# Kernel optimization log

Measured on AMD Instinct MI355X. Metric: run time of the kernel, lower is better.

## Reference

```python
import jax, jax.numpy as jnp
import numpy as np
jax.config.update("jax_enable_x64", True)

T, C, F = 2048, 2048, 8192
f32 = jnp.float32
f64 = jnp.float64


def setup_inputs() -> dict:
    key = jax.random.key(0)
    ks = jax.random.split(key, 20)
    s = 0.02
    return {
        "x": jax.random.normal(ks[0], (T, C), f32),
        "att_shift": jnp.zeros((C,), f32),
        "wkv_state": jnp.zeros((2, C), f32),
        "ffn_shift": jnp.zeros((C,), f32),
        "ln1_w": jnp.ones((C,), f32),
        "ln1_b": jnp.zeros((C,), f32),
        "ln2_w": jnp.ones((C,), f32),
        "ln2_b": jnp.zeros((C,), f32),
        "time_mix_k": jax.random.uniform(ks[1], (C,), f32),
        "time_mix_v": jax.random.uniform(ks[2], (C,), f32),
        "time_mix_r": jax.random.uniform(ks[3], (C,), f32),
        "time_decay": jax.random.normal(ks[4], (C,), f32) * 0.5,
        "time_first": jax.random.normal(ks[5], (C,), f32) * 0.5,
        "att_key": jax.random.normal(ks[6], (C, C), f32) * s,
        "att_value": jax.random.normal(ks[7], (C, C), f32) * s,
        "att_receptance": jax.random.normal(ks[8], (C, C), f32) * s,
        "att_output": jax.random.normal(ks[9], (C, C), f32) * s,
        "ffn_time_mix_k": jax.random.uniform(ks[10], (C,), f32),
        "ffn_time_mix_r": jax.random.uniform(ks[11], (C,), f32),
        "ffn_key": jax.random.normal(ks[12], (F, C), f32) * s,
        "ffn_value": jax.random.normal(ks[13], (C, F), f32) * s,
        "ffn_receptance": jax.random.normal(ks[14], (C, C), f32) * s,
    }


def _ln(x, w, b):
    m = x.mean(-1, keepdims=True)
    v = x.var(-1, keepdims=True)
    return (x - m) * jax.lax.rsqrt(v + 1e-5) * w + b


def _wkv(time_decay, time_first, k, v, wkv_state):
    # faithful to wkv_mop: double-precision math, float32 state round-trip per step
    u = time_first.astype(f64)
    w = -jnp.exp(time_decay.astype(f64))
    ew = jnp.exp(w)

    def step(carry, kv_t):
        a, b = carry  # float32 states [C]
        k_t, v_t = kv_t
        kd = k_t.astype(f64)
        vd = v_t.astype(f64)
        e = jnp.exp(u + w + kd)
        y = (a + e * vd) / (b + e)
        kk = jnp.exp(kd)
        a2 = ((a + kk * vd) * ew).astype(f32)
        b2 = ((b + kk) * ew).astype(f32)
        return (a2, b2), y.astype(f32)

    _, y = jax.lax.scan(step, (wkv_state[0], wkv_state[1]), (k, v))
    return y  # [T, C]


def reference(x, att_shift, wkv_state, ffn_shift, ln1_w, ln1_b, ln2_w, ln2_b,
              time_mix_k, time_mix_v, time_mix_r, time_decay, time_first,
              att_key, att_value, att_receptance, att_output,
              ffn_time_mix_k, ffn_time_mix_r, ffn_key, ffn_value, ffn_receptance):
    # --- TimeMix (att) on rx = ln1(x); shiftamount=2 -> prev token of rx ---
    rx = _ln(x, ln1_w, ln1_b)                         # [T, C]
    xx = jnp.concatenate([att_shift[None, :], rx[:-1]], axis=0)
    xk = rx * time_mix_k + xx * (1.0 - time_mix_k)
    xv = rx * time_mix_v + xx * (1.0 - time_mix_v)
    xr = rx * time_mix_r + xx * (1.0 - time_mix_r)
    k = xk @ att_key.T                                # [T, C]
    v = xv @ att_value.T
    sr = jax.nn.sigmoid(xr @ att_receptance.T)
    y = _wkv(time_decay, time_first, k, v, wkv_state)
    x = x + (sr * y) @ att_output.T
    # --- ChannelMix (ffn) on fx = ln2(x); shift = prev token of fx ---
    fx = _ln(x, ln2_w, ln2_b)
    fxx = jnp.concatenate([ffn_shift[None, :], fx[:-1]], axis=0)
    fk = fx * ffn_time_mix_k + fxx * (1.0 - ffn_time_mix_k)
    fr = fx * ffn_time_mix_r + fxx * (1.0 - ffn_time_mix_r)
    kf = jnp.square(jax.nn.relu(fk @ ffn_key.T))      # [T, F]
    kv = kf @ ffn_value.T                             # [T, C]
    out = x + jax.nn.sigmoid(fr @ ffn_receptance.T) * kv
    return out
```

## Files before the change

kernel.cpp:

```cpp
#include <hip/hip_runtime.h>
#include <hip/hip_bf16.h>

typedef unsigned short u16;
typedef short bf16x8 __attribute__((ext_vector_type(8)));
typedef float f32x4 __attribute__((ext_vector_type(4)));

#define T_DIM 2048
#define C_DIM 2048
#define F_DIM 8192
#define WKV_L 32
#define WKV_P (T_DIM / WKV_L)

__device__ __forceinline__ u16 f2bf(float f) {
    unsigned int u = __float_as_uint(f);
    u += 0x7fff + ((u >> 16) & 1);
    return (u16)(u >> 16);
}

__device__ __forceinline__ void async16(const void* g, void* l) {
    __builtin_amdgcn_global_load_lds(
        (__attribute__((address_space(1))) const unsigned int*)g,
        (__attribute__((address_space(3))) unsigned int*)l, 16, 0, 0);
}

__global__ __launch_bounds__(256) void ln_mix3(
        const float* __restrict__ x, const float* __restrict__ sh,
        const float* __restrict__ w, const float* __restrict__ b,
        const float* __restrict__ mk, const float* __restrict__ mv,
        const float* __restrict__ mr,
        u16* __restrict__ xk, u16* __restrict__ xv, u16* __restrict__ xr) {
    __shared__ float red[16];
    const int t = blockIdx.x, tid = threadIdx.x;
    const float4* cr = (const float4*)(x + (size_t)t * C_DIM);
    float4 c0 = cr[tid * 2], c1 = cr[tid * 2 + 1];
    float s = c0.x + c0.y + c0.z + c0.w + c1.x + c1.y + c1.z + c1.w;
    float q = c0.x * c0.x + c0.y * c0.y + c0.z * c0.z + c0.w * c0.w
            + c1.x * c1.x + c1.y * c1.y + c1.z * c1.z + c1.w * c1.w;
    float4 p0, p1;
    float sp = 0.f, qp = 0.f;
    if (t > 0) {
        const float4* pr = (const float4*)(x + (size_t)(t - 1) * C_DIM);
        p0 = pr[tid * 2]; p1 = pr[tid * 2 + 1];
        sp = p0.x + p0.y + p0.z + p0.w + p1.x + p1.y + p1.z + p1.w;
        qp = p0.x * p0.x + p0.y * p0.y + p0.z * p0.z + p0.w * p0.w
           + p1.x * p1.x + p1.y * p1.y + p1.z * p1.z + p1.w * p1.w;
    } else {
        const float4* pr = (const float4*)sh;
        p0 = pr[tid * 2]; p1 = pr[tid * 2 + 1];
    }
    #pragma unroll
    for (int off = 32; off > 0; off >>= 1) {
        s += __shfl_down(s, off);   q += __shfl_down(q, off);
        sp += __shfl_down(sp, off); qp += __shfl_down(qp, off);
    }
    const int lane = tid & 63, wv = tid >> 6;
    if (lane == 0) { red[wv] = s; red[4 + wv] = q; red[8 + wv] = sp; red[12 + wv] = qp; }
    __syncthreads();
    if (tid == 0) {
        red[0] += red[1] + red[2] + red[3];
        red[4] += red[5] + red[6] + red[7];
        red[8] += red[9] + red[10] + red[11];
        red[12] += red[13] + red[14] + red[15];
    }
    __syncthreads();
    const float mc = red[0] * (1.f / C_DIM);
    const float ic = rsqrtf(red[4] * (1.f / C_DIM) - mc * mc + 1e-5f);
    const float mp = red[8] * (1.f / C_DIM);
    const float ip = rsqrtf(red[12] * (1.f / C_DIM) - mp * mp + 1e-5f);
    const float4* w4 = (const float4*)w;
    const float4* b4 = (const float4*)b;
    #pragma unroll
    for (int j = 0; j < 2; ++j) {
        const int i4 = tid * 2 + j;
        float4 cv = j ? c1 : c0, pv = j ? p1 : p0;
        float4 wv4 = w4[i4], bv = b4[i4];
        float4 cl, pl;
        cl.x = (cv.x - mc) * ic * wv4.x + bv.x;
        cl.y = (cv.y - mc) * ic * wv4.y + bv.y;
        cl.z = (cv.z - mc) * ic * wv4.z + bv.z;
        cl.w = (cv.w - mc) * ic * wv4.w + bv.w;
        if (t > 0) {
            pl.x = (pv.x - mp) * ip * wv4.x + bv.x;
            pl.y = (pv.y - mp) * ip * wv4.y + bv.y;
            pl.z = (pv.z - mp) * ip * wv4.z + bv.z;
            pl.w = (pv.w - mp) * ip * wv4.w + bv.w;
        } else pl = pv;
        const size_t o = (size_t)t * (C_DIM / 4) + i4;
        float4 m;
        ushort4 r;
        m = ((const float4*)mk)[i4];
        r.x = f2bf(cl.x * m.x + pl.x * (1.f - m.x));
        r.y = f2bf(cl.y * m.y + pl.y * (1.f - m.y));
        r.z = f2bf(cl.z * m.z + pl.z * (1.f - m.z));
        r.w = f2bf(cl.w * m.w + pl.w * (1.f - m.w));
        ((ushort4*)xk)[o] = r;
        m = ((const float4*)mv)[i4];
        r.x = f2bf(cl.x * m.x + pl.x * (1.f - m.x));
        r.y = f2bf(cl.y * m.y + pl.y * (1.f - m.y));
        r.z = f2bf(cl.z * m.z + pl.z * (1.f - m.z));
        r.w = f2bf(cl.w * m.w + pl.w * (1.f - m.w));
        ((ushort4*)xv)[o] = r;
        m = ((const float4*)mr)[i4];
        r.x = f2bf(cl.x * m.x + pl.x * (1.f - m.x));
        r.y = f2bf(cl.y * m.y + pl.y * (1.f - m.y));
        r.z = f2bf(cl.z * m.z + pl.z * (1.f - m.z));
        r.w = f2bf(cl.w * m.w + pl.w * (1.f - m.w));
        ((ushort4*)xr)[o] = r;
    }
}

__global__ __launch_bounds__(256) void ln_mix2(
        const float* __restrict__ x, const float* __restrict__ sh,
        const float* __restrict__ w, const float* __restrict__ b,
        const float* __restrict__ mk, const float* __restrict__ mr,
        u16* __restrict__ fk, u16* __restrict__ fr) {
    __shared__ float red[16];
    const int t = blockIdx.x, tid = threadIdx.x;
    const float4* cr = (const float4*)(x + (size_t)t * C_DIM);
    float4 c0 = cr[tid * 2], c1 = cr[tid * 2 + 1];
    float s = c0.x + c0.y + c0.z + c0.w + c1.x + c1.y + c1.z + c1.w;
    float q = c0.x * c0.x + c0.y * c0.y + c0.z * c0.z + c0.w * c0.w
            + c1.x * c1.x + c1.y * c1.y + c1.z * c1.z + c1.w * c1.w;
    float4 p0, p1;
    float sp = 0.f, qp = 0.f;
    if (t > 0) {
        const float4* pr = (const float4*)(x + (size_t)(t - 1) * C_DIM);
        p0 = pr[tid * 2]; p1 = pr[tid * 2 + 1];
        sp = p0.x + p0.y + p0.z + p0.w + p1.x + p1.y + p1.z + p1.w;
        qp = p0.x * p0.x + p0.y * p0.y + p0.z * p0.z + p0.w * p0.w
           + p1.x * p1.x + p1.y * p1.y + p1.z * p1.z + p1.w * p1.w;
    } else {
        const float4* pr = (const float4*)sh;
        p0 = pr[tid * 2]; p1 = pr[tid * 2 + 1];
    }
    #pragma unroll
    for (int off = 32; off > 0; off >>= 1) {
        s += __shfl_down(s, off);   q += __shfl_down(q, off);
        sp += __shfl_down(sp, off); qp += __shfl_down(qp, off);
    }
    const int lane = tid & 63, wv = tid >> 6;
    if (lane == 0) { red[wv] = s; red[4 + wv] = q; red[8 + wv] = sp; red[12 + wv] = qp; }
    __syncthreads();
    if (tid == 0) {
        red[0] += red[1] + red[2] + red[3];
        red[4] += red[5] + red[6] + red[7];
        red[8] += red[9] + red[10] + red[11];
        red[12] += red[13] + red[14] + red[15];
    }
    __syncthreads();
    const float mc = red[0] * (1.f / C_DIM);
    const float ic = rsqrtf(red[4] * (1.f / C_DIM) - mc * mc + 1e-5f);
    const float mp = red[8] * (1.f / C_DIM);
    const float ip = rsqrtf(red[12] * (1.f / C_DIM) - mp * mp + 1e-5f);
    const float4* w4 = (const float4*)w;
    const float4* b4 = (const float4*)b;
    #pragma unroll
    for (int j = 0; j < 2; ++j) {
        const int i4 = tid * 2 + j;
        float4 cv = j ? c1 : c0, pv = j ? p1 : p0;
        float4 wv4 = w4[i4], bv = b4[i4];
        float4 cl, pl;
        cl.x = (cv.x - mc) * ic * wv4.x + bv.x;
        cl.y = (cv.y - mc) * ic * wv4.y + bv.y;
        cl.z = (cv.z - mc) * ic * wv4.z + bv.z;
        cl.w = (cv.w - mc) * ic * wv4.w + bv.w;
        if (t > 0) {
            pl.x = (pv.x - mp) * ip * wv4.x + bv.x;
            pl.y = (pv.y - mp) * ip * wv4.y + bv.y;
            pl.z = (pv.z - mp) * ip * wv4.z + bv.z;
            pl.w = (pv.w - mp) * ip * wv4.w + bv.w;
        } else pl = pv;
        const size_t o = (size_t)t * (C_DIM / 4) + i4;
        float4 m;
        ushort4 r;
        m = ((const float4*)mk)[i4];
        r.x = f2bf(cl.x * m.x + pl.x * (1.f - m.x));
        r.y = f2bf(cl.y * m.y + pl.y * (1.f - m.y));
        r.z = f2bf(cl.z * m.z + pl.z * (1.f - m.z));
        r.w = f2bf(cl.w * m.w + pl.w * (1.f - m.w));
        ((ushort4*)fk)[o] = r;
        m = ((const float4*)mr)[i4];
        r.x = f2bf(cl.x * m.x + pl.x * (1.f - m.x));
        r.y = f2bf(cl.y * m.y + pl.y * (1.f - m.y));
        r.z = f2bf(cl.z * m.z + pl.z * (1.f - m.z));
        r.w = f2bf(cl.w * m.w + pl.w * (1.f - m.w));
        ((ushort4*)fr)[o] = r;
    }
}

__global__ __launch_bounds__(256) void cvt_bf16(const float* __restrict__ in,
                                                u16* __restrict__ out, int n8) {
    int i = blockIdx.x * 256 + threadIdx.x;
    const int stride = gridDim.x * 256;
    for (; i < n8; i += stride) {
        const float4* p = (const float4*)(in + (size_t)i * 8);
        float4 a = p[0], b = p[1];
        ushort4 lo, hi;
        lo.x = f2bf(a.x); lo.y = f2bf(a.y); lo.z = f2bf(a.z); lo.w = f2bf(a.w);
        hi.x = f2bf(b.x); hi.y = f2bf(b.y); hi.z = f2bf(b.z); hi.w = f2bf(b.w);
        ((ushort4*)out)[i * 2] = lo;
        ((ushort4*)out)[i * 2 + 1] = hi;
    }
}

__global__ __launch_bounds__(256) void cvt3_bf16(const float* __restrict__ i0,
                                                 const float* __restrict__ i1,
                                                 const float* __restrict__ i2,
                                                 u16* __restrict__ out, int n8) {
    const int sel = blockIdx.y;
    const float* in = sel == 0 ? i0 : (sel == 1 ? i1 : i2);
    u16* o = out + (size_t)sel * n8 * 8;
    int i = blockIdx.x * 256 + threadIdx.x;
    const int stride = gridDim.x * 256;
    for (; i < n8; i += stride) {
        const float4* p = (const float4*)(in + (size_t)i * 8);
        float4 a = p[0], b = p[1];
        ushort4 lo, hi;
        lo.x = f2bf(a.x); lo.y = f2bf(a.y); lo.z = f2bf(a.z); lo.w = f2bf(a.w);
        hi.x = f2bf(b.x); hi.y = f2bf(b.y); hi.z = f2bf(b.z); hi.w = f2bf(b.w);
        ((ushort4*)o)[i * 2] = lo;
        ((ushort4*)o)[i * 2 + 1] = hi;
    }
}

__global__ __launch_bounds__(256) void wkv_part(const float* __restrict__ td,
                                                const float* __restrict__ k,
                                                const float* __restrict__ v,
                                                float* __restrict__ Ab,
                                                float* __restrict__ Bb) {
    const int idx = blockIdx.x * 256 + threadIdx.x;
    const int c = idx & (C_DIM - 1);
    const int p = idx >> 11;
    const float ew = expf(-expf(td[c]));
    float A = 0.f, B = 0.f;
    size_t o = (size_t)(p * WKV_L) * C_DIM + c;
    #pragma unroll 4
    for (int i = 0; i < WKV_L; ++i, o += C_DIM) {
        const float kk = expf(k[o]);
        A = (A + kk * v[o]) * ew;
        B = (B + kk) * ew;
    }
    Ab[p * C_DIM + c] = A;
    Bb[p * C_DIM + c] = B;
}

__global__ __launch_bounds__(256) void wkv_comb(const float* __restrict__ td,
                                                const float* __restrict__ st,
                                                const float* __restrict__ Ab,
                                                const float* __restrict__ Bb,
                                                float* __restrict__ Sa,
                                                float* __restrict__ Sb) {
    const int c = blockIdx.x * 256 + threadIdx.x;
    const float w = -expf(td[c]);
    const float dL = expf(w * (float)WKV_L);
    float a = st[c];
    float b = st[C_DIM + c];
    #pragma unroll 4
    for (int p = 0; p < WKV_P; ++p) {
        Sa[p * C_DIM + c] = a;
        Sb[p * C_DIM + c] = b;
        a = dL * a + Ab[p * C_DIM + c];
        b = dL * b + Bb[p * C_DIM + c];
    }
}

__global__ __launch_bounds__(256) void wkv_emit(const float* __restrict__ td,
                                                const float* __restrict__ tf,
                                                const float* __restrict__ k,
                                                const float* __restrict__ v,
                                                const float* __restrict__ r,
                                                const float* __restrict__ Sa,
                                                const float* __restrict__ Sb,
                                                u16* __restrict__ pout) {
    const int idx = blockIdx.x * 256 + threadIdx.x;
    const int c = idx & (C_DIM - 1);
    const int p = idx >> 11;
    const float u = tf[c];
    const float w = -expf(td[c]);
    const float ew = expf(w);
    float a = Sa[p * C_DIM + c];
    float b = Sb[p * C_DIM + c];
    size_t o = (size_t)(p * WKV_L) * C_DIM + c;
    #pragma unroll 2
    for (int i = 0; i < WKV_L; ++i, o += C_DIM) {
        const float kt = k[o], vt = v[o], rt = r[o];
        const float e = expf(u + w + kt);
        const float y = (a + e * vt) / (b + e);
        const float kk = expf(kt);
        a = (a + kk * vt) * ew;
        b = (b + kk) * ew;
        const float sr = 1.f / (1.f + expf(-rt));
        pout[o] = f2bf(sr * y);
    }
}

enum { EPI_F32 = 0, EPI_ADDX = 1, EPI_RELU2 = 2, EPI_SIGMULADD4 = 3 };

template <int EPI>
__global__ __launch_bounds__(512, 2) void gemm256(
        const u16* __restrict__ A, int lda, long a_zs,
        const u16* __restrict__ B, int ldb, long b_zs,
        int Kloop,
        void* __restrict__ outp, int ldo, long o_zs,
        const float* __restrict__ aux1, const float* __restrict__ aux2) {
    __shared__ u16 lds[4 * 16384];
    const int tid = threadIdx.x;
    const int l = tid & 63, w = tid >> 6;
    const int wr = w >> 2, wcn = w & 3;

    const int gx = gridDim.x, gy = gridDim.y;
    const int nxy = gx * gy;
    const int flat = (blockIdx.z * gy + blockIdx.y) * gx + blockIdx.x;
    const int cpx = (nxy * gridDim.z) >> 3;
    const int swz = (flat & 7) * cpx + (flat >> 3);
    const int z = swz / nxy;
    const int rem = swz - z * nxy;
    const int bm = rem % gy;
    const int bn = rem / gy;

    const u16* Ag = A + (size_t)z * a_zs + (size_t)bm * 256 * lda;
    const u16* Bg = B + (size_t)z * b_zs + (size_t)bn * 256 * ldb;

    long gA[2], gB[2];
    int dA[2], dB[2];
    #pragma unroll
    for (int j = 0; j < 2; ++j) {
        const int off = j * 8192 + w * 1024 + l * 16;
        const int row = off >> 6;
        const int cb = (off & 63) ^ (((off >> 9) & 1) << 5);
        gA[j] = (long)row * lda + (cb >> 1);
        gB[j] = (long)row * ldb + (cb >> 1);
        dA[j] = j * 4096 + w * 512;
        dB[j] = 8192 + j * 4096 + w * 512;
    }

    int offA[8], offB[4];
    #pragma unroll
    for (int m = 0; m < 8; ++m) {
        const int lin = (wr * 128 + m * 16 + (l & 15)) * 64 + ((l >> 4) << 4);
        offA[m] = (lin ^ (((lin >> 9) & 1) << 5)) >> 1;
    }
    #pragma unroll
    for (int n = 0; n < 4; ++n) {
        const int lin = (wcn * 64 + n * 16 + (l & 15)) * 64 + ((l >> 4) << 4);
        offB[n] = 8192 + ((lin ^ (((lin >> 9) & 1) << 5)) >> 1);
    }

    const f32x4 fz = {0.f, 0.f, 0.f, 0.f};
    f32x4 acc[8][4];
    #pragma unroll
    for (int m = 0; m < 8; ++m)
        #pragma unroll
        for (int n = 0; n < 4; ++n) acc[m][n] = fz;

    const int NT = Kloop >> 5;

    auto stage = [&](int kt, int sp) {
        const long ko = (long)kt << 5;
        const int sb = sp * 16384;
        async16(Ag + gA[0] + ko, &lds[sb + dA[0]]);
        async16(Ag + gA[1] + ko, &lds[sb + dA[1]]);
        async16(Bg + gB[0] + ko, &lds[sb + dB[0]]);
        async16(Bg + gB[1] + ko, &lds[sb + dB[1]]);
    };

    stage(0, 0);
    stage(1, 1);
    stage(2, 2);

    for (int t = 0; t < NT; ++t) {
        asm volatile("s_waitcnt vmcnt(8)" ::: "memory");
        __builtin_amdgcn_s_barrier();
        __builtin_amdgcn_sched_barrier(0);
        {
            const int tp = (t + 3 < NT) ? t + 3 : NT - 1;
            stage(tp, (t + 3) & 3);
        }
        const int sb = (t & 3) * 16384;
        bf16x8 af[8], bfv[4];
        #pragma unroll
        for (int m = 0; m < 8; ++m) af[m] = *(const bf16x8*)&lds[sb + offA[m]];
        #pragma unroll
        for (int n = 0; n < 4; ++n) bfv[n] = *(const bf16x8*)&lds[sb + offB[n]];
        __builtin_amdgcn_s_setprio(1);
        #pragma unroll
        for (int m = 0; m < 4; ++m)
            #pragma unroll
            for (int n = 0; n < 4; ++n)
                acc[m][n] = __builtin_amdgcn_mfma_f32_16x16x32_bf16(af[m], bfv[n], acc[m][n], 0, 0, 0);
        __builtin_amdgcn_s_setprio(0);
        __builtin_amdgcn_s_setprio(1);
        #pragma unroll
        for (int m = 4; m < 8; ++m)
            #pragma unroll
            for (int n = 0; n < 4; ++n)
                acc[m][n] = __builtin_amdgcn_mfma_f32_16x16x32_bf16(af[m], bfv[n], acc[m][n], 0, 0, 0);
        __builtin_amdgcn_s_setprio(0);
    }
    asm volatile("s_waitcnt vmcnt(0)" ::: "memory");

    const int r00 = bm * 256 + wr * 128 + ((l >> 4) << 2);
    const int c00 = bn * 256 + wcn * 64 + (l & 15);
    #pragma unroll
    for (int m = 0; m < 8; ++m) {
        #pragma unroll
        for (int n = 0; n < 4; ++n) {
            #pragma unroll
            for (int j = 0; j < 4; ++j) {
                const int rr = r00 + m * 16 + j;
                const int cc = c00 + n * 16;
                const size_t o = (size_t)rr * ldo + cc;
                const float val = acc[m][n][j];
                if constexpr (EPI == EPI_F32) {
                    ((float*)outp)[(size_t)z * o_zs + o] = val;
                } else if constexpr (EPI == EPI_ADDX) {
                    ((float*)outp)[o] = aux1[o] + val;
                } else if constexpr (EPI == EPI_RELU2) {
                    const float tp2 = fmaxf(val, 0.f);
                    ((u16*)outp)[o] = f2bf(tp2 * tp2);
                } else {
                    const float kv = aux2[o]
                                   + aux2[o + (size_t)T_DIM * C_DIM]
                                   + aux2[o + 2 * (size_t)T_DIM * C_DIM]
                                   + aux2[o + 3 * (size_t)T_DIM * C_DIM];
                    const float sg = 1.f / (1.f + expf(-val));
                    ((float*)outp)[o] = aux1[o] + sg * kv;
                }
            }
        }
    }
}

extern "C" void kernel_launch(void* const* d_in, const int* in_sizes, int n_in,
                              void* d_out, int out_size, void* d_ws, size_t ws_size,
                              hipStream_t stream) {
    const float* x         = (const float*)d_in[0];
    const float* att_shift = (const float*)d_in[1];
    const float* wkv_state = (const float*)d_in[2];
    const float* ffn_shift = (const float*)d_in[3];
    const float* ln1w = (const float*)d_in[4];
    const float* ln1b = (const float*)d_in[5];
    const float* ln2w = (const float*)d_in[6];
    const float* ln2b = (const float*)d_in[7];
    const float* tmk  = (const float*)d_in[8];
    const float* tmv  = (const float*)d_in[9];
    const float* tmr  = (const float*)d_in[10];
    const float* td   = (const float*)d_in[11];
    const float* tf   = (const float*)d_in[12];
    const float* Wk   = (const float*)d_in[13];
    const float* Wv   = (const float*)d_in[14];
    const float* Wr   = (const float*)d_in[15];
    const float* Wo   = (const float*)d_in[16];
    const float* ftmk = (const float*)d_in[17];
    const float* ftmr = (const float*)d_in[18];
    const float* Wfk  = (const float*)d_in[19];
    const float* Wfv  = (const float*)d_in[20];
    const float* Wfr  = (const float*)d_in[21];
    float* out = (float*)d_out;

    char* ws = (char*)d_ws;
    const size_t MB = 1ull << 20;
    u16*   xk  = (u16*)(ws + 16 * MB);
    u16*   xv  = (u16*)(ws + 24 * MB);
    u16*   xr  = (u16*)(ws + 32 * MB);
    float* kb  = (float*)(ws + 40 * MB);
    float* vb  = (float*)(ws + 56 * MB);
    float* rb  = (float*)(ws + 72 * MB);
    u16*   pb  = (u16*)(ws + 88 * MB);
    float* x1  = (float*)(ws + 96 * MB);
    u16*   kf  = (u16*)(ws + 112 * MB);
    u16*   Wb  = (u16*)(ws + 144 * MB);
    float* wAb = (float*)(ws + 112 * MB);
    float* wBb = (float*)(ws + 112 * MB + 512 * 1024);
    float* wSa = (float*)(ws + 113 * MB);
    float* wSb = (float*)(ws + 113 * MB + 512 * 1024);
    float* fvp = (float*)(ws + 32 * MB);

    const int T = T_DIM, C = C_DIM, F = F_DIM;
    const dim3 blk(256), blk5(512);

    ln_mix3<<<T, blk, 0, stream>>>(x, att_shift, ln1w, ln1b, tmk, tmv, tmr, xk, xv, xr);

    cvt3_bf16<<<dim3(1024, 3), blk, 0, stream>>>(Wk, Wv, Wr, Wb, C * C / 8);
    gemm256<EPI_F32><<<dim3(C / 256, T / 256, 3), blk5, 0, stream>>>(
        xk, C, (long)T * C, Wb, C, (long)C * C, C, kb, C, (long)T * C, nullptr, nullptr);

    wkv_part<<<(C * WKV_P) / 256, blk, 0, stream>>>(td, kb, vb, wAb, wBb);
    wkv_comb<<<C / 256, blk, 0, stream>>>(td, wkv_state, wAb, wBb, wSa, wSb);
    wkv_emit<<<(C * WKV_P) / 256, blk, 0, stream>>>(td, tf, kb, vb, rb, wSa, wSb, pb);

    cvt_bf16<<<2048, blk, 0, stream>>>(Wo, Wb, C * C / 8);
    gemm256<EPI_ADDX><<<dim3(C / 256, T / 256, 1), blk5, 0, stream>>>(
        pb, C, 0, Wb, C, 0, C, x1, C, 0, x, nullptr);

    ln_mix2<<<T, blk, 0, stream>>>(x1, ffn_shift, ln2w, ln2b, ftmk, ftmr, xk, xv);

    cvt_bf16<<<2048, blk, 0, stream>>>(Wfk, Wb, F * C / 8);
    gemm256<EPI_RELU2><<<dim3(F / 256, T / 256, 1), blk5, 0, stream>>>(
        xk, C, 0, Wb, C, 0, C, kf, F, 0, nullptr, nullptr);

    cvt_bf16<<<2048, blk, 0, stream>>>(Wfv, Wb, C * F / 8);
    gemm256<EPI_F32><<<dim3(C / 256, T / 256, 4), blk5, 0, stream>>>(
        kf, F, 2048, Wb, F, 2048, 2048, fvp, C, (long)T * C, nullptr, nullptr);

    cvt_bf16<<<2048, blk, 0, stream>>>(Wfr, Wb, C * C / 8);
    gemm256<EPI_SIGMULADD4><<<dim3(C / 256, T / 256, 1), blk5, 0, stream>>>(
        xv, C, 0, Wb, C, 0, C, out, C, 0, x1, fvp);
}
```

Baseline: 451.6 us.

## Use 128x128 GEMM kernel for square projections and pre-reduce split-K partials

```diff
diff --git a/kernel.cpp b/kernel.cpp
--- a/kernel.cpp
+++ b/kernel.cpp
@@ -223,6 +223,25 @@
     }
 }
 
+__global__ __launch_bounds__(256) void reduce4(const float* __restrict__ p0,
+                                               const float* __restrict__ p1,
+                                               const float* __restrict__ p2,
+                                               const float* __restrict__ p3,
+                                               float* __restrict__ o, int n4) {
+    int i = blockIdx.x * 256 + threadIdx.x;
+    const int stride = gridDim.x * 256;
+    for (; i < n4; i += stride) {
+        float4 a = ((const float4*)p0)[i], b = ((const float4*)p1)[i];
+        float4 c = ((const float4*)p2)[i], d = ((const float4*)p3)[i];
+        float4 r;
+        r.x = a.x + b.x + c.x + d.x;
+        r.y = a.y + b.y + c.y + d.y;
+        r.z = a.z + b.z + c.z + d.z;
+        r.w = a.w + b.w + c.w + d.w;
+        ((float4*)o)[i] = r;
+    }
+}
+
 __global__ __launch_bounds__(256) void wkv_part(const float* __restrict__ td,
                                                 const float* __restrict__ k,
                                                 const float* __restrict__ v,
@@ -294,7 +313,7 @@
     }
 }
 
-enum { EPI_F32 = 0, EPI_ADDX = 1, EPI_RELU2 = 2, EPI_SIGMULADD4 = 3 };
+enum { EPI_F32 = 0, EPI_ADDX = 1, EPI_RELU2 = 2, EPI_SIGMULADD = 3 };
 
 template <int EPI>
 __global__ __launch_bounds__(512, 2) void gemm256(
@@ -413,18 +432,90 @@
                 const float val = acc[m][n][j];
                 if constexpr (EPI == EPI_F32) {
                     ((float*)outp)[(size_t)z * o_zs + o] = val;
-                } else if constexpr (EPI == EPI_ADDX) {
-                    ((float*)outp)[o] = aux1[o] + val;
-                } else if constexpr (EPI == EPI_RELU2) {
+                } else {
                     const float tp2 = fmaxf(val, 0.f);
                     ((u16*)outp)[o] = f2bf(tp2 * tp2);
+                }
+            }
+        }
+    }
+}
+
+template <int EPI>
+__global__ __launch_bounds__(256) void gemm_bt(const u16* __restrict__ A,
+                                               const u16* __restrict__ B,
+                                               int M, int N, int K,
+                                               void* __restrict__ outp,
+                                               const float* __restrict__ aux1,
+                                               const float* __restrict__ aux2) {
+    __shared__ u16 As[128 * 64];
+    __shared__ u16 Bs[128 * 64];
+    const int tid = threadIdx.x;
+    const int lane = tid & 63, wid = tid >> 6;
+    const int wr = wid >> 1, wc = wid & 1;
+    const int bm = blockIdx.y, bn = blockIdx.x;
+
+    const u16* Ag = A + (size_t)bm * 128 * K;
+    const u16* Bg = B + (size_t)bn * 128 * K;
+
+    const f32x4 fz = {0.f, 0.f, 0.f, 0.f};
+    f32x4 acc[4][4];
+    #pragma unroll
+    for (int m = 0; m < 4; ++m)
+        #pragma unroll
+        for (int n = 0; n < 4; ++n) acc[m][n] = fz;
+
+    const int nk = K >> 6;
+    for (int kt = 0; kt < nk; ++kt) {
+        const u16* Agk = Ag + (kt << 6);
+        const u16* Bgk = Bg + (kt << 6);
+        #pragma unroll
+        for (int i = 0; i < 4; ++i) {
+            const int id = i * 256 + tid;
+            async16(Agk + (size_t)(id >> 3) * K + ((id & 7) << 3), &As[(i * 4 + wid) << 9]);
+        }
+        #pragma unroll
+        for (int i = 0; i < 4; ++i) {
+            const int id = i * 256 + tid;
+            async16(Bgk + (size_t)(id >> 3) * K + ((id & 7) << 3), &Bs[(i * 4 + wid) << 9]);
+        }
+        __syncthreads();
+        #pragma unroll
+        for (int kk = 0; kk < 2; ++kk) {
+            const int ko = (kk << 5) + ((lane >> 4) << 3);
+            bf16x8 af[4], bfr[4];
+            #pragma unroll
+            for (int m = 0; m < 4; ++m)
+                af[m] = *(const bf16x8*)&As[((wr << 6) + (m << 4) + (lane & 15)) * 64 + ko];
+            #pragma unroll
+            for (int n = 0; n < 4; ++n)
+                bfr[n] = *(const bf16x8*)&Bs[((wc << 6) + (n << 4) + (lane & 15)) * 64 + ko];
+            #pragma unroll
+            for (int m = 0; m < 4; ++m)
+                #pragma unroll
+                for (int n = 0; n < 4; ++n)
+                    acc[m][n] = __builtin_amdgcn_mfma_f32_16x16x32_bf16(af[m], bfr[n], acc[m][n], 0, 0, 0);
+        }
+        __syncthreads();
+    }
+
+    const int r0 = bm * 128 + (wr << 6) + ((lane >> 4) << 2);
+    const int c0 = bn * 128 + (wc << 6) + (lane & 15);
+    #pragma unroll
+    for (int m = 0; m < 4; ++m) {
+        #pragma unroll
+        for (int n = 0; n < 4; ++n) {
+            #pragma unroll
+            for (int j = 0; j < 4; ++j) {
+                const int rr = r0 + (m << 4) + j;
+                const int cc = c0 + (n << 4);
+                const size_t o = (size_t)rr * N + cc;
+                const float val = acc[m][n][j];
+                if constexpr (EPI == EPI_ADDX) {
+                    ((float*)outp)[o] = aux1[o] + val;
                 } else {
-                    const float kv = aux2[o]
-                                   + aux2[o + (size_t)T_DIM * C_DIM]
-                                   + aux2[o + 2 * (size_t)T_DIM * C_DIM]
-                                   + aux2[o + 3 * (size_t)T_DIM * C_DIM];
                     const float sg = 1.f / (1.f + expf(-val));
-                    ((float*)outp)[o] = aux1[o] + sg * kv;
+                    ((float*)outp)[o] = aux1[o] + sg * aux2[o];
                 }
             }
         }
@@ -460,6 +551,7 @@
 
     char* ws = (char*)d_ws;
     const size_t MB = 1ull << 20;
+    float* rx0 = (float*)(ws + 0);
     u16*   xk  = (u16*)(ws + 16 * MB);
     u16*   xv  = (u16*)(ws + 24 * MB);
     u16*   xr  = (u16*)(ws + 32 * MB);
@@ -490,8 +582,8 @@
     wkv_emit<<<(C * WKV_P) / 256, blk, 0, stream>>>(td, tf, kb, vb, rb, wSa, wSb, pb);
 
     cvt_bf16<<<2048, blk, 0, stream>>>(Wo, Wb, C * C / 8);
-    gemm256<EPI_ADDX><<<dim3(C / 256, T / 256, 1), blk5, 0, stream>>>(
-        pb, C, 0, Wb, C, 0, C, x1, C, 0, x, nullptr);
+    gemm_bt<EPI_ADDX><<<dim3(C / 128, T / 128), blk, 0, stream>>>(
+        pb, Wb, T, C, C, x1, x, nullptr);
 
     ln_mix2<<<T, blk, 0, stream>>>(x1, ffn_shift, ln2w, ln2b, ftmk, ftmr, xk, xv);
 
@@ -502,8 +594,10 @@
     cvt_bf16<<<2048, blk, 0, stream>>>(Wfv, Wb, C * F / 8);
     gemm256<EPI_F32><<<dim3(C / 256, T / 256, 4), blk5, 0, stream>>>(
         kf, F, 2048, Wb, F, 2048, 2048, fvp, C, (long)T * C, nullptr, nullptr);
+    reduce4<<<2048, blk, 0, stream>>>(fvp, fvp + (size_t)T * C, fvp + 2 * (size_t)T * C,
+                                      fvp + 3 * (size_t)T * C, rx0, T * C / 4);
 
     cvt_bf16<<<2048, blk, 0, stream>>>(Wfr, Wb, C * C / 8);
-    gemm256<EPI_SIGMULADD4><<<dim3(C / 256, T / 256, 1), blk5, 0, stream>>>(
-        xv, C, 0, Wb, C, 0, C, out, C, 0, x1, fvp);
-}
+    gemm_bt<EPI_SIGMULADD><<<dim3(C / 128, T / 128), blk, 0, stream>>>(
+        xv, Wb, T, C, C, out, x1, rx0);
+}
```

Result: faster. 421.8 us (-6.6%).

## Shrink GEMM tiles to 128x128 and use two-way split-K with separate reduction

Applied to the files above, without the earlier changes.

```diff
diff --git a/kernel.cpp b/kernel.cpp
--- a/kernel.cpp
+++ b/kernel.cpp
@@ -223,6 +223,22 @@
     }
 }
 
+__global__ __launch_bounds__(256) void reduce2(const float* __restrict__ p0,
+                                               const float* __restrict__ p1,
+                                               float* __restrict__ o, int n4) {
+    int i = blockIdx.x * 256 + threadIdx.x;
+    const int stride = gridDim.x * 256;
+    for (; i < n4; i += stride) {
+        float4 a = ((const float4*)p0)[i], b = ((const float4*)p1)[i];
+        float4 r;
+        r.x = a.x + b.x;
+        r.y = a.y + b.y;
+        r.z = a.z + b.z;
+        r.w = a.w + b.w;
+        ((float4*)o)[i] = r;
+    }
+}
+
 __global__ __launch_bounds__(256) void wkv_part(const float* __restrict__ td,
                                                 const float* __restrict__ k,
                                                 const float* __restrict__ v,
@@ -294,19 +310,19 @@
     }
 }
 
-enum { EPI_F32 = 0, EPI_ADDX = 1, EPI_RELU2 = 2, EPI_SIGMULADD4 = 3 };
+enum { EPI_F32 = 0, EPI_ADDX = 1, EPI_RELU2 = 2, EPI_SIGMULADD = 3 };
 
 template <int EPI>
-__global__ __launch_bounds__(512, 2) void gemm256(
+__global__ __launch_bounds__(256, 2) void gemm_bt(
         const u16* __restrict__ A, int lda, long a_zs,
         const u16* __restrict__ B, int ldb, long b_zs,
-        int Kloop,
+        long koff, int Kloop,
         void* __restrict__ outp, int ldo, long o_zs,
         const float* __restrict__ aux1, const float* __restrict__ aux2) {
-    __shared__ u16 lds[4 * 16384];
+    __shared__ u16 lds[4 * 8192];
     const int tid = threadIdx.x;
     const int l = tid & 63, w = tid >> 6;
-    const int wr = w >> 2, wcn = w & 3;
+    const int wr2 = w >> 1, wc2 = w & 1;
 
     const int gx = gridDim.x, gy = gridDim.y;
     const int nxy = gx * gy;
@@ -318,38 +334,38 @@
     const int bm = rem % gy;
     const int bn = rem / gy;
 
-    const u16* Ag = A + (size_t)z * a_zs + (size_t)bm * 256 * lda;
-    const u16* Bg = B + (size_t)z * b_zs + (size_t)bn * 256 * ldb;
+    const u16* Ag = A + (size_t)z * a_zs + (size_t)z * koff + (size_t)bm * 128 * lda;
+    const u16* Bg = B + (size_t)z * b_zs + (size_t)z * koff + (size_t)bn * 128 * ldb;
 
     long gA[2], gB[2];
     int dA[2], dB[2];
     #pragma unroll
     for (int j = 0; j < 2; ++j) {
-        const int off = j * 8192 + w * 1024 + l * 16;
+        const int off = j * 4096 + w * 1024 + l * 16;
         const int row = off >> 6;
         const int cb = (off & 63) ^ (((off >> 9) & 1) << 5);
         gA[j] = (long)row * lda + (cb >> 1);
         gB[j] = (long)row * ldb + (cb >> 1);
-        dA[j] = j * 4096 + w * 512;
-        dB[j] = 8192 + j * 4096 + w * 512;
-    }
-
-    int offA[8], offB[4];
-    #pragma unroll
-    for (int m = 0; m < 8; ++m) {
-        const int lin = (wr * 128 + m * 16 + (l & 15)) * 64 + ((l >> 4) << 4);
+        dA[j] = j * 2048 + w * 512;
+        dB[j] = 4096 + j * 2048 + w * 512;
+    }
+
+    int offA[4], offB[4];
+    #pragma unroll
+    for (int m = 0; m < 4; ++m) {
+        const int lin = (wr2 * 64 + m * 16 + (l & 15)) * 64 + ((l >> 4) << 4);
         offA[m] = (lin ^ (((lin >> 9) & 1) << 5)) >> 1;
     }
     #pragma unroll
     for (int n = 0; n < 4; ++n) {
-        const int lin = (wcn * 64 + n * 16 + (l & 15)) * 64 + ((l >> 4) << 4);
-        offB[n] = 8192 + ((lin ^ (((lin >> 9) & 1) << 5)) >> 1);
+        const int lin = (wc2 * 64 + n * 16 + (l & 15)) * 64 + ((l >> 4) << 4);
+        offB[n] = 4096 + ((lin ^ (((lin >> 9) & 1) << 5)) >> 1);
     }
 
     const f32x4 fz = {0.f, 0.f, 0.f, 0.f};
-    f32x4 acc[8][4];
-    #pragma unroll
-    for (int m = 0; m < 8; ++m)
+    f32x4 acc[4][4];
+    #pragma unroll
+    for (int m = 0; m < 4; ++m)
         #pragma unroll
         for (int n = 0; n < 4; ++n) acc[m][n] = fz;
 
@@ -357,7 +373,7 @@
 
     auto stage = [&](int kt, int sp) {
         const long ko = (long)kt << 5;
-        const int sb = sp * 16384;
+        const int sb = sp * 8192;
         async16(Ag + gA[0] + ko, &lds[sb + dA[0]]);
         async16(Ag + gA[1] + ko, &lds[sb + dA[1]]);
         async16(Bg + gB[0] + ko, &lds[sb + dB[0]]);
@@ -376,22 +392,22 @@
             const int tp = (t + 3 < NT) ? t + 3 : NT - 1;
             stage(tp, (t + 3) & 3);
         }
-        const int sb = (t & 3) * 16384;
-        bf16x8 af[8], bfv[4];
+        const int sb = (t & 3) * 8192;
+        bf16x8 af[4], bfv[4];
         #pragma unroll
-        for (int m = 0; m < 8; ++m) af[m] = *(const bf16x8*)&lds[sb + offA[m]];
+        for (int m = 0; m < 4; ++m) af[m] = *(const bf16x8*)&lds[sb + offA[m]];
         #pragma unroll
         for (int n = 0; n < 4; ++n) bfv[n] = *(const bf16x8*)&lds[sb + offB[n]];
         __builtin_amdgcn_s_setprio(1);
         #pragma unroll
-        for (int m = 0; m < 4; ++m)
+        for (int m = 0; m < 2; ++m)
             #pragma unroll
             for (int n = 0; n < 4; ++n)
                 acc[m][n] = __builtin_amdgcn_mfma_f32_16x16x32_bf16(af[m], bfv[n], acc[m][n], 0, 0, 0);
         __builtin_amdgcn_s_setprio(0);
         __builtin_amdgcn_s_setprio(1);
         #pragma unroll
-        for (int m = 4; m < 8; ++m)
+        for (int m = 2; m < 4; ++m)
             #pragma unroll
             for (int n = 0; n < 4; ++n)
                 acc[m][n] = __builtin_amdgcn_mfma_f32_16x16x32_bf16(af[m], bfv[n], acc[m][n], 0, 0, 0);
@@ -399,10 +415,10 @@
     }
     asm volatile("s_waitcnt vmcnt(0)" ::: "memory");
 
-    const int r00 = bm * 256 + wr * 128 + ((l >> 4) << 2);
-    const int c00 = bn * 256 + wcn * 64 + (l & 15);
-    #pragma unroll
-    for (int m = 0; m < 8; ++m) {
+    const int r00 = bm * 128 + wr2 * 64 + ((l >> 4) << 2);
+    const int c00 = bn * 128 + wc2 * 64 + (l & 15);
+    #pragma unroll
+    for (int m = 0; m < 4; ++m) {
         #pragma unroll
         for (int n = 0; n < 4; ++n) {
             #pragma unroll
@@ -419,12 +435,8 @@
                     const float tp2 = fmaxf(val, 0.f);
                     ((u16*)outp)[o] = f2bf(tp2 * tp2);
                 } else {
-                    const float kv = aux2[o]
-                                   + aux2[o + (size_t)T_DIM * C_DIM]
-                                   + aux2[o + 2 * (size_t)T_DIM * C_DIM]
-                                   + aux2[o + 3 * (size_t)T_DIM * C_DIM];
                     const float sg = 1.f / (1.f + expf(-val));
-                    ((float*)outp)[o] = aux1[o] + sg * kv;
+                    ((float*)outp)[o] = aux1[o] + sg * aux2[o];
                 }
             }
         }
@@ -460,6 +472,7 @@
 
     char* ws = (char*)d_ws;
     const size_t MB = 1ull << 20;
+    float* rx0 = (float*)(ws + 0);
     u16*   xk  = (u16*)(ws + 16 * MB);
     u16*   xv  = (u16*)(ws + 24 * MB);
     u16*   xr  = (u16*)(ws + 32 * MB);
@@ -477,33 +490,35 @@
     float* fvp = (float*)(ws + 32 * MB);
 
     const int T = T_DIM, C = C_DIM, F = F_DIM;
-    const dim3 blk(256), blk5(512);
+    const dim3 blk(256);
 
     ln_mix3<<<T, blk, 0, stream>>>(x, att_shift, ln1w, ln1b, tmk, tmv, tmr, xk, xv, xr);
 
     cvt3_bf16<<<dim3(1024, 3), blk, 0, stream>>>(Wk, Wv, Wr, Wb, C * C / 8);
-    gemm256<EPI_F32><<<dim3(C / 256, T / 256, 3), blk5, 0, stream>>>(
-        xk, C, (long)T * C, Wb, C, (long)C * C, C, kb, C, (long)T * C, nullptr, nullptr);
+    gemm_bt<EPI_F32><<<dim3(C / 128, T / 128, 3), blk, 0, stream>>>(
+        xk, C, (long)T * C, Wb, C, (long)C * C, 0, C,
+        kb, C, (long)T * C, nullptr, nullptr);
 
     wkv_part<<<(C * WKV_P) / 256, blk, 0, stream>>>(td, kb, vb, wAb, wBb);
     wkv_comb<<<C / 256, blk, 0, stream>>>(td, wkv_state, wAb, wBb, wSa, wSb);
     wkv_emit<<<(C * WKV_P) / 256, blk, 0, stream>>>(td, tf, kb, vb, rb, wSa, wSb, pb);
 
     cvt_bf16<<<2048, blk, 0, stream>>>(Wo, Wb, C * C / 8);
-    gemm256<EPI_ADDX><<<dim3(C / 256, T / 256, 1), blk5, 0, stream>>>(
-        pb, C, 0, Wb, C, 0, C, x1, C, 0, x, nullptr);
+    gemm_bt<EPI_ADDX><<<dim3(C / 128, T / 128, 1), blk, 0, stream>>>(
+        pb, C, 0, Wb, C, 0, 0, C, x1, C, 0, x, nullptr);
 
     ln_mix2<<<T, blk, 0, stream>>>(x1, ffn_shift, ln2w, ln2b, ftmk, ftmr, xk, xv);
 
     cvt_bf16<<<2048, blk, 0, stream>>>(Wfk, Wb, F * C / 8);
-    gemm256<EPI_RELU2><<<dim3(F / 256, T / 256, 1), blk5, 0, stream>>>(
-        xk, C, 0, Wb, C, 0, C, kf, F, 0, nullptr, nullptr);
+    gemm_bt<EPI_RELU2><<<dim3(F / 128, T / 128, 1), blk, 0, stream>>>(
+        xk, C, 0, Wb, C, 0, 0, C, kf, F, 0, nullptr, nullptr);
 
     cvt_bf16<<<2048, blk, 0, stream>>>(Wfv, Wb, C * F / 8);
-    gemm256<EPI_F32><<<dim3(C / 256, T / 256, 4), blk5, 0, stream>>>(
-        kf, F, 2048, Wb, F, 2048, 2048, fvp, C, (long)T * C, nullptr, nullptr);
+    gemm_bt<EPI_F32><<<dim3(C / 128, T / 128, 2), blk, 0, stream>>>(
+        kf, F, 0, Wb, F, 0, 4096, 4096, fvp, C, (long)T * C, nullptr, nullptr);
+    reduce2<<<2048, blk, 0, stream>>>(fvp, fvp + (size_t)T * C, rx0, T * C / 4);
 
     cvt_bf16<<<2048, blk, 0, stream>>>(Wfr, Wb, C * C / 8);
-    gemm256<EPI_SIGMULADD4><<<dim3(C / 256, T / 256, 1), blk5, 0, stream>>>(
-        xv, C, 0, Wb, C, 0, C, out, C, 0, x1, fvp);
-}
+    gemm_bt<EPI_SIGMULADD><<<dim3(C / 128, T / 128, 1), blk, 0, stream>>>(
+        xv, C, 0, Wb, C, 0, 0, C, out, C, 0, x1, rx0);
+}
```

Result: faster. 410.0 us (-9.2%).
